# Kernel tuning notes

Hardware: AMD Instinct MI355X
Metric: run time of the kernel (lower is better)

Reference implementation:

```python
import jax, jax.numpy as jnp
import numpy as np
from jax.scipy.special import logsumexp

# Complete binary tree, heap indexing: node i has children 2i+1, 2i+2.
# Edge for child c (c >= 1) is edge_pot[c-1], shape [C, C]:
#   rows = parent state, cols = child state (matches torch code's
#   logsumexp(edge + msg, dim=1) upward and edge.T downward).
DEPTH = 18
C = 16
N = 2 ** (DEPTH + 1) - 1  # 524287 nodes, N-1 edges


def setup_inputs() -> dict:
    key = jax.random.key(0)
    k1, k2 = jax.random.split(key)
    unary = jax.random.normal(k1, (N, C), dtype=jnp.float32)
    edge_pot = jax.random.normal(k2, (N - 1, C, C), dtype=jnp.float32)
    return {"unary": unary, "edge_pot": edge_pot, "depth": DEPTH}


def reference(unary, edge_pot, depth):
    """Sum-product belief propagation on a complete binary tree.

    Returns beliefs [N, C]: for each node v,
      belief[v] = unary[v] + sum(up messages from children) + down message from parent,
    identical to the per-message torch BFS loop, but processed level-parallel.
    """
    c = unary.shape[1]
    # ---------- upward pass (leaves -> root) ----------
    # subtotal[v] = unary[v] + sum of up-messages from v's children (V2F to parent factor)
    subtotal = unary
    m_up = jnp.zeros_like(unary)  # m_up[ch] = F2V message from edge (parent, ch) to parent
    for d in range(depth, 0, -1):
        lo, hi = 2 ** d - 1, 2 ** (d + 1) - 1          # children level, size 2^d
        ep = edge_pot[lo - 1:hi - 1]                    # [2^d, C, C]
        # logsumexp over child state (axis 2): torch's logsumexp(edge + msg, dim=1)
        msg = logsumexp(ep + subtotal[lo:hi][:, None, :], axis=2)  # [2^d, C]
        m_up = m_up.at[lo:hi].set(msg)
        plo, phi = 2 ** (d - 1) - 1, 2 ** d - 1
        # children of consecutive parents are consecutive pairs (2p+1, 2p+2)
        subtotal = subtotal.at[plo:phi].add(msg.reshape(-1, 2, c).sum(axis=1))
    # ---------- downward pass (root -> leaves) ----------
    m_down = jnp.zeros_like(unary)  # m_down[ch] = F2V message from edge (parent, ch) to ch
    for d in range(1, depth + 1):
        lo, hi = 2 ** d - 1, 2 ** (d + 1) - 1
        plo, phi = 2 ** (d - 1) - 1, 2 ** d - 1
        # V2F from parent p towards child ch: all incoming F2V at p except m_up[ch]
        par_total = jnp.repeat(subtotal[plo:phi] + m_down[plo:phi], 2, axis=0)  # [2^d, C]
        v2f = par_total - m_up[lo:hi]
        ep_t = jnp.swapaxes(edge_pot[lo - 1:hi - 1], 1, 2)  # edge.T: [2^d, Cchild, Cparent]
        msg = logsumexp(ep_t + v2f[:, None, :], axis=2)     # logsumexp over parent state
        m_down = m_down.at[lo:hi].set(msg)
    return subtotal + m_down  # beliefs [N, C]
```

## Files before the change

### kernel.cpp

```cpp
#include <hip/hip_runtime.h>
#include <stdint.h>


#ifndef __has_builtin
#define __has_builtin(x) 0
#endif
#if __has_builtin(__builtin_amdgcn_cvt_pk_fp8_f32) && __has_builtin(__builtin_amdgcn_cvt_f32_fp8)
#define EP8_FP8 1
#define EPC_BYTES 256
#else
#define EP8_FP8 0
#define EPC_BYTES 512
#endif

__device__ __forceinline__ void ldvec16(const float* p, float* d) {
    const float4* q = (const float4*)p;
    #pragma unroll
    for (int t = 0; t < 4; ++t) {
        float4 a = q[t];
        d[4*t+0] = a.x; d[4*t+1] = a.y; d[4*t+2] = a.z; d[4*t+3] = a.w;
    }
}

__device__ __forceinline__ float lse16_rs(const float* r, const float* s) {
    float v[16];
    float m;
    #pragma unroll
    for (int j = 0; j < 16; ++j) {
        v[j] = r[j] + s[j];
        m = (j == 0) ? v[0] : fmaxf(m, v[j]);
    }
    float acc = 0.f;
    #pragma unroll
    for (int j = 0; j < 16; ++j) acc += __expf(v[j] - m);
    return m + __logf(acc);
}

__device__ __forceinline__ void enc_row(uint8_t* dst, const float* r) {
#if EP8_FP8
    int w[4];
    #pragma unroll
    for (int t = 0; t < 4; ++t) {
        int x = __builtin_amdgcn_cvt_pk_fp8_f32(r[4*t+0], r[4*t+1], 0, false);
        x     = __builtin_amdgcn_cvt_pk_fp8_f32(r[4*t+2], r[4*t+3], x, true);
        w[t] = x;
    }
    *(int4*)dst = make_int4(w[0], w[1], w[2], w[3]);
#else
    uint32_t w[8];
    #pragma unroll
    for (int t = 0; t < 8; ++t) {
        uint32_t lo = __float_as_uint(r[2*t+0]);
        uint32_t hi = __float_as_uint(r[2*t+1]);
        w[t] = (lo >> 16) | (hi & 0xffff0000u);
    }
    ((int4*)dst)[0] = make_int4(w[0], w[1], w[2], w[3]);
    ((int4*)dst)[1] = make_int4(w[4], w[5], w[6], w[7]);
#endif
}

__device__ __forceinline__ void dec_row(const uint8_t* src, float* r) {
#if EP8_FP8
    uint4 w = *(const uint4*)src;
    uint32_t ws[4] = {w.x, w.y, w.z, w.w};
    #pragma unroll
    for (int t = 0; t < 4; ++t) {
        uint32_t u = ws[t];
        r[4*t+0] = __builtin_amdgcn_cvt_f32_fp8(u, 0);
        r[4*t+1] = __builtin_amdgcn_cvt_f32_fp8(u, 1);
        r[4*t+2] = __builtin_amdgcn_cvt_f32_fp8(u, 2);
        r[4*t+3] = __builtin_amdgcn_cvt_f32_fp8(u, 3);
    }
#else
    uint4 w0 = ((const uint4*)src)[0];
    uint4 w1 = ((const uint4*)src)[1];
    uint32_t ws[8] = {w0.x, w0.y, w0.z, w0.w, w1.x, w1.y, w1.z, w1.w};
    #pragma unroll
    for (int t = 0; t < 8; ++t) {
        r[2*t+0] = __uint_as_float(ws[t] << 16);
        r[2*t+1] = __uint_as_float(ws[t] & 0xffff0000u);
    }
#endif
}

__device__ __forceinline__ float dec_elem(const uint8_t* nodebase, int k, int i) {
#if EP8_FP8
    return __builtin_amdgcn_cvt_f32_fp8((uint32_t)nodebase[k*16 + i], 0);
#else
    uint32_t u = ((const uint16_t*)nodebase)[k*16 + i];
    return __uint_as_float(u << 16);
#endif
}

template <bool WRITE8>
__device__ __forceinline__ void up_body(const float* csrc, const float* __restrict__ unary,
                                        const float* __restrict__ ep, float* out,
                                        uint8_t* __restrict__ e8, int p, int i) {
    int cl = 2*p + 1, cr = cl + 1;
    float s[16], r[16];

    ldvec16(csrc + (size_t)cl*16, s);
    ldvec16(ep + (size_t)(cl-1)*256 + i*16, r);
    float msgL = lse16_rs(r, s);
    if (WRITE8) enc_row(e8 + (size_t)(cl-1)*EPC_BYTES + i*(EPC_BYTES/16), r);

    ldvec16(csrc + (size_t)cr*16, s);
    ldvec16(ep + (size_t)(cr-1)*256 + i*16, r);
    float msgR = lse16_rs(r, s);
    if (WRITE8) enc_row(e8 + (size_t)(cr-1)*EPC_BYTES + i*(EPC_BYTES/16), r);

    out[(size_t)p*16 + i] = unary[(size_t)p*16 + i] + msgL + msgR;
}

template <bool READ8>
__device__ __forceinline__ void down_body(const float* subsrc, const float* __restrict__ ep,
                                          const uint8_t* __restrict__ e8, float* out,
                                          int v, int i) {
    int par = (v - 1) >> 1;
    float s[16], r[16];
    ldvec16(subsrc + (size_t)v*16, s);
    float sub_i = subsrc[(size_t)v*16 + i];

    if (READ8) dec_row(e8 + (size_t)(v-1)*EPC_BYTES + i*(EPC_BYTES/16), r);
    else       ldvec16(ep + (size_t)(v-1)*256 + i*16, r);
    float mup = lse16_rs(r, s);

    float pt  = out[(size_t)par*16 + i];
    float v2f = pt - mup;

    float c[16];
    if (READ8) {
        const uint8_t* nb = e8 + (size_t)(v-1)*EPC_BYTES;
        #pragma unroll
        for (int k = 0; k < 16; ++k) c[k] = dec_elem(nb, k, i);
    } else {
        const float* nb = ep + (size_t)(v-1)*256 + i;
        #pragma unroll
        for (int k = 0; k < 16; ++k) c[k] = nb[k*16];
    }

    float vv[16], m;
    #pragma unroll
    for (int k = 0; k < 16; ++k) {
        float t = c[k] + __shfl(v2f, k, 16);
        vv[k] = t;
        m = (k == 0) ? t : fmaxf(m, t);
    }
    float acc = 0.f;
    #pragma unroll
    for (int k = 0; k < 16; ++k) acc += __expf(vv[k] - m);
    float msg = m + __logf(acc);

    out[(size_t)v*16 + i] = sub_i + msg;
}

template <bool WRITE8>
__global__ __launch_bounds__(256) void up_k(const float* csrc, const float* __restrict__ unary,
                                            const float* __restrict__ ep, float* out,
                                            uint8_t* __restrict__ e8, int plo, int pcount) {
    int t = blockIdx.x * blockDim.x + threadIdx.x;
    if (t >= pcount * 16) return;
    up_body<WRITE8>(csrc, unary, ep, out, e8, plo + (t >> 4), t & 15);
}

template <bool READ8>
__global__ __launch_bounds__(256) void down_k(const float* subsrc, const float* __restrict__ ep,
                                              const uint8_t* __restrict__ e8, float* out,
                                              int lo, int count) {
    int t = blockIdx.x * blockDim.x + threadIdx.x;
    if (t >= count * 16) return;
    down_body<READ8>(subsrc, ep, e8, out, lo + (t >> 4), t & 15);
}

__global__ __launch_bounds__(1024) void top_fused(const float* __restrict__ unary,
                                                  const float* __restrict__ ep,
                                                  float* out, int FD) {
    int tid = threadIdx.x;
    for (int d = FD; d >= 1; --d) {
        int pcount = 1 << (d - 1);
        int plo = pcount - 1;
        int total = pcount * 16;
        for (int t = tid; t < total; t += blockDim.x)
            up_body<false>(out, unary, ep, out, nullptr, plo + (t >> 4), t & 15);
        __syncthreads();
    }
    for (int d = 1; d <= FD; ++d) {
        int count = 1 << d;
        int lo = count - 1;
        int total = count * 16;
        for (int t = tid; t < total; t += blockDim.x)
            down_body<false>(out, ep, nullptr, out, lo + (t >> 4), t & 15);
        __syncthreads();
    }
}

extern "C" void kernel_launch(void* const* d_in, const int* in_sizes, int n_in,
                              void* d_out, int out_size, void* d_ws, size_t ws_size,
                              hipStream_t stream) {
    const float* unary = (const float*)d_in[0];
    const float* ep    = (const float*)d_in[1];
    float* out = (float*)d_out;
    uint8_t* e8 = (uint8_t*)d_ws;

    int Nn = in_sizes[0] / 16;
    int depth = 0;
    while ((1 << (depth + 1)) < Nn + 1) ++depth;

    bool use8 = ws_size >= (size_t)(Nn - 1) * EPC_BYTES;
    int FD = (depth >= 7) ? 6 : 0;

    for (int d = depth; d >= FD + 1; --d) {
        int pcount = 1 << (d - 1);
        int plo = pcount - 1;
        const float* csrc = (d == depth) ? unary : out;
        int threads = pcount * 16;
        dim3 grid((threads + 255) / 256), block(256);
        if (use8) up_k<true ><<<grid, block, 0, stream>>>(csrc, unary, ep, out, e8, plo, pcount);
        else      up_k<false><<<grid, block, 0, stream>>>(csrc, unary, ep, out, e8, plo, pcount);
    }

    if (FD > 0)
        top_fused<<<1, 1024, 0, stream>>>(unary, ep, out, FD);

    for (int d = FD + 1; d <= depth; ++d) {
        int count = 1 << d;
        int lo = count - 1;
        const float* subsrc = (d == depth) ? unary : out;
        int threads = count * 16;
        dim3 grid((threads + 255) / 256), block(256);
        if (use8) down_k<true ><<<grid, block, 0, stream>>>(subsrc, ep, e8, out, lo, count);
        else      down_k<false><<<grid, block, 0, stream>>>(subsrc, ep, e8, out, lo, count);
    }
}
```

Before: 279.8 us.

## Fuse six tree levels per kernel using per-block subtrees with shared-memory handoff

```diff
diff --git a/kernel.cpp b/kernel.cpp
--- a/kernel.cpp
+++ b/kernel.cpp
@@ -92,84 +92,146 @@
 #endif
 }
 
-template <bool WRITE8>
-__device__ __forceinline__ void up_body(const float* csrc, const float* __restrict__ unary,
-                                        const float* __restrict__ ep, float* out,
-                                        uint8_t* __restrict__ e8, int p, int i) {
-    int cl = 2*p + 1, cr = cl + 1;
+template <bool USE8>
+__global__ __launch_bounds__(256) void up_sub(
+    const float* __restrict__ unary, const float* __restrict__ ep,
+    float* __restrict__ out, uint8_t* __restrict__ e8,
+    int rl, int dl, int depth) {
+    __shared__ float sub[2][32][16];
+    int j = blockIdx.x;
+    int cur = 0;
+    for (int d = dl; d > rl; --d) {
+        int np = 1 << (d - 1 - rl);
+        size_t pbase = (((size_t)1 << (d - 1)) - 1) + (size_t)j * np;
+        bool fromGlobal = (d == dl);
+        const float* gsrc = (d == depth) ? unary : out;
+        for (int t = threadIdx.x; t < np * 16; t += 256) {
+            int pl = t >> 4, i = t & 15;
+            size_t p = pbase + pl;
+            size_t cl = 2 * p + 1, cr = cl + 1;
+            float s[16], r[16];
+
+            if (fromGlobal) ldvec16(gsrc + cl * 16, s);
+            else            ldvec16(&sub[cur ^ 1][2 * pl][0], s);
+            ldvec16(ep + (cl - 1) * 256 + i * 16, r);
+            float msgL = lse16_rs(r, s);
+            if (USE8) enc_row(e8 + (cl - 1) * EPC_BYTES + i * (EPC_BYTES / 16), r);
+
+            if (fromGlobal) ldvec16(gsrc + cr * 16, s);
+            else            ldvec16(&sub[cur ^ 1][2 * pl + 1][0], s);
+            ldvec16(ep + (cr - 1) * 256 + i * 16, r);
+            float msgR = lse16_rs(r, s);
+            if (USE8) enc_row(e8 + (cr - 1) * EPC_BYTES + i * (EPC_BYTES / 16), r);
+
+            float v = unary[p * 16 + i] + msgL + msgR;
+            out[p * 16 + i] = v;
+            if (d - 1 > rl) sub[cur][pl][i] = v;
+        }
+        __syncthreads();
+        cur ^= 1;
+    }
+}
+
+template <bool USE8>
+__global__ __launch_bounds__(256) void down_sub(
+    const float* __restrict__ unary, const float* __restrict__ ep,
+    const uint8_t* __restrict__ e8, float* __restrict__ out,
+    int rl, int dl, int depth) {
+    __shared__ float bel[2][32][16];
+    int j = blockIdx.x;
+    int cur = 0;
+    for (int d = rl + 1; d <= dl; ++d) {
+        int nc = 1 << (d - rl);
+        size_t cbase = (((size_t)1 << d) - 1) + (size_t)j * nc;
+        bool leaf = (d == depth);
+        bool parGlobal = (d == rl + 1);
+        for (int t = threadIdx.x; t < nc * 16; t += 256) {
+            int vl = t >> 4, i = t & 15;
+            size_t v = cbase + vl;
+            const float* ssrc = leaf ? unary : out;
+            float s[16], r[16];
+            ldvec16(ssrc + v * 16, s);
+            float sub_i = ssrc[v * 16 + i];
+
+            if (USE8) dec_row(e8 + (v - 1) * EPC_BYTES + i * (EPC_BYTES / 16), r);
+            else      ldvec16(ep + (v - 1) * 256 + i * 16, r);
+            float mup = lse16_rs(r, s);
+
+            float pt;
+            if (parGlobal) pt = out[((v - 1) >> 1) * 16 + i];
+            else           pt = bel[cur ^ 1][vl >> 1][i];
+            float v2f = pt - mup;
+
+            float c[16];
+            if (USE8) {
+                const uint8_t* nb = e8 + (v - 1) * EPC_BYTES;
+                #pragma unroll
+                for (int k = 0; k < 16; ++k) c[k] = dec_elem(nb, k, i);
+            } else {
+                const float* nb = ep + (v - 1) * 256 + i;
+                #pragma unroll
+                for (int k = 0; k < 16; ++k) c[k] = nb[k * 16];
+            }
+
+            float vv[16], m;
+            #pragma unroll
+            for (int k = 0; k < 16; ++k) {
+                float x = c[k] + __shfl(v2f, k, 16);
+                vv[k] = x;
+                m = (k == 0) ? x : fmaxf(m, x);
+            }
+            float acc = 0.f;
+            #pragma unroll
+            for (int k = 0; k < 16; ++k) acc += __expf(vv[k] - m);
+            float msg = m + __logf(acc);
+
+            float b = sub_i + msg;
+            out[v * 16 + i] = b;
+            if (d < dl) bel[cur][vl][i] = b;
+        }
+        __syncthreads();
+        cur ^= 1;
+    }
+}
+
+__device__ __forceinline__ void up_body_f32(const float* __restrict__ unary,
+                                            const float* __restrict__ ep,
+                                            float* out, size_t p, int i) {
+    size_t cl = 2 * p + 1, cr = cl + 1;
     float s[16], r[16];
-
-    ldvec16(csrc + (size_t)cl*16, s);
-    ldvec16(ep + (size_t)(cl-1)*256 + i*16, r);
+    ldvec16(out + cl * 16, s);
+    ldvec16(ep + (cl - 1) * 256 + i * 16, r);
     float msgL = lse16_rs(r, s);
-    if (WRITE8) enc_row(e8 + (size_t)(cl-1)*EPC_BYTES + i*(EPC_BYTES/16), r);
-
-    ldvec16(csrc + (size_t)cr*16, s);
-    ldvec16(ep + (size_t)(cr-1)*256 + i*16, r);
+    ldvec16(out + cr * 16, s);
+    ldvec16(ep + (cr - 1) * 256 + i * 16, r);
     float msgR = lse16_rs(r, s);
-    if (WRITE8) enc_row(e8 + (size_t)(cr-1)*EPC_BYTES + i*(EPC_BYTES/16), r);
-
-    out[(size_t)p*16 + i] = unary[(size_t)p*16 + i] + msgL + msgR;
-}
-
-template <bool READ8>
-__device__ __forceinline__ void down_body(const float* subsrc, const float* __restrict__ ep,
-                                          const uint8_t* __restrict__ e8, float* out,
-                                          int v, int i) {
-    int par = (v - 1) >> 1;
+    out[p * 16 + i] = unary[p * 16 + i] + msgL + msgR;
+}
+
+__device__ __forceinline__ void down_body_f32(const float* __restrict__ ep,
+                                              float* out, size_t v, int i) {
+    size_t par = (v - 1) >> 1;
     float s[16], r[16];
-    ldvec16(subsrc + (size_t)v*16, s);
-    float sub_i = subsrc[(size_t)v*16 + i];
-
-    if (READ8) dec_row(e8 + (size_t)(v-1)*EPC_BYTES + i*(EPC_BYTES/16), r);
-    else       ldvec16(ep + (size_t)(v-1)*256 + i*16, r);
+    ldvec16(out + v * 16, s);
+    float sub_i = out[v * 16 + i];
+    ldvec16(ep + (v - 1) * 256 + i * 16, r);
     float mup = lse16_rs(r, s);
-
-    float pt  = out[(size_t)par*16 + i];
-    float v2f = pt - mup;
-
+    float v2f = out[par * 16 + i] - mup;
+    const float* nb = ep + (v - 1) * 256 + i;
     float c[16];
-    if (READ8) {
-        const uint8_t* nb = e8 + (size_t)(v-1)*EPC_BYTES;
-        #pragma unroll
-        for (int k = 0; k < 16; ++k) c[k] = dec_elem(nb, k, i);
-    } else {
-        const float* nb = ep + (size_t)(v-1)*256 + i;
-        #pragma unroll
-        for (int k = 0; k < 16; ++k) c[k] = nb[k*16];
-    }
-
+    #pragma unroll
+    for (int k = 0; k < 16; ++k) c[k] = nb[k * 16];
     float vv[16], m;
     #pragma unroll
     for (int k = 0; k < 16; ++k) {
-        float t = c[k] + __shfl(v2f, k, 16);
-        vv[k] = t;
-        m = (k == 0) ? t : fmaxf(m, t);
+        float x = c[k] + __shfl(v2f, k, 16);
+        vv[k] = x;
+        m = (k == 0) ? x : fmaxf(m, x);
     }
     float acc = 0.f;
     #pragma unroll
     for (int k = 0; k < 16; ++k) acc += __expf(vv[k] - m);
-    float msg = m + __logf(acc);
-
-    out[(size_t)v*16 + i] = sub_i + msg;
-}
-
-template <bool WRITE8>
-__global__ __launch_bounds__(256) void up_k(const float* csrc, const float* __restrict__ unary,
-                                            const float* __restrict__ ep, float* out,
-                                            uint8_t* __restrict__ e8, int plo, int pcount) {
-    int t = blockIdx.x * blockDim.x + threadIdx.x;
-    if (t >= pcount * 16) return;
-    up_body<WRITE8>(csrc, unary, ep, out, e8, plo + (t >> 4), t & 15);
-}
-
-template <bool READ8>
-__global__ __launch_bounds__(256) void down_k(const float* subsrc, const float* __restrict__ ep,
-                                              const uint8_t* __restrict__ e8, float* out,
-                                              int lo, int count) {
-    int t = blockIdx.x * blockDim.x + threadIdx.x;
-    if (t >= count * 16) return;
-    down_body<READ8>(subsrc, ep, e8, out, lo + (t >> 4), t & 15);
+    out[v * 16 + i] = sub_i + m + __logf(acc);
 }
 
 __global__ __launch_bounds__(1024) void top_fused(const float* __restrict__ unary,
@@ -178,18 +240,16 @@
     int tid = threadIdx.x;
     for (int d = FD; d >= 1; --d) {
         int pcount = 1 << (d - 1);
-        int plo = pcount - 1;
-        int total = pcount * 16;
-        for (int t = tid; t < total; t += blockDim.x)
-            up_body<false>(out, unary, ep, out, nullptr, plo + (t >> 4), t & 15);
+        size_t plo = pcount - 1;
+        for (int t = tid; t < pcount * 16; t += blockDim.x)
+            up_body_f32(unary, ep, out, plo + (t >> 4), t & 15);
         __syncthreads();
     }
     for (int d = 1; d <= FD; ++d) {
         int count = 1 << d;
-        int lo = count - 1;
-        int total = count * 16;
-        for (int t = tid; t < total; t += blockDim.x)
-            down_body<false>(out, ep, nullptr, out, lo + (t >> 4), t & 15);
+        size_t lo = count - 1;
+        for (int t = tid; t < count * 16; t += blockDim.x)
+            down_body_f32(ep, out, lo + (t >> 4), t & 15);
         __syncthreads();
     }
 }
@@ -207,28 +267,26 @@
     while ((1 << (depth + 1)) < Nn + 1) ++depth;
 
     bool use8 = ws_size >= (size_t)(Nn - 1) * EPC_BYTES;
-    int FD = (depth >= 7) ? 6 : 0;
-
-    for (int d = depth; d >= FD + 1; --d) {
-        int pcount = 1 << (d - 1);
-        int plo = pcount - 1;
-        const float* csrc = (d == depth) ? unary : out;
-        int threads = pcount * 16;
-        dim3 grid((threads + 255) / 256), block(256);
-        if (use8) up_k<true ><<<grid, block, 0, stream>>>(csrc, unary, ep, out, e8, plo, pcount);
-        else      up_k<false><<<grid, block, 0, stream>>>(csrc, unary, ep, out, e8, plo, pcount);
-    }
-
+
+    int rls[8], dls[8], nch = 0;
+    int dl = depth;
+    if (depth > 6) {
+        while (dl > 6) { rls[nch] = dl - 6; dls[nch] = dl; ++nch; dl -= 6; }
+    } else {
+        rls[0] = 0; dls[0] = depth; nch = 1; dl = 0;
+    }
+    int FD = dl;
+
+    for (int c = 0; c < nch; ++c) {
+        dim3 grid(1u << rls[c]), block(256);
+        if (use8) up_sub<true ><<<grid, block, 0, stream>>>(unary, ep, out, e8, rls[c], dls[c], depth);
+        else      up_sub<false><<<grid, block, 0, stream>>>(unary, ep, out, e8, rls[c], dls[c], depth);
+    }
     if (FD > 0)
         top_fused<<<1, 1024, 0, stream>>>(unary, ep, out, FD);
-
-    for (int d = FD + 1; d <= depth; ++d) {
-        int count = 1 << d;
-        int lo = count - 1;
-        const float* subsrc = (d == depth) ? unary : out;
-        int threads = count * 16;
-        dim3 grid((threads + 255) / 256), block(256);
-        if (use8) down_k<true ><<<grid, block, 0, stream>>>(subsrc, ep, e8, out, lo, count);
-        else      down_k<false><<<grid, block, 0, stream>>>(subsrc, ep, e8, out, lo, count);
-    }
-}
+    for (int c = nch - 1; c >= 0; --c) {
+        dim3 grid(1u << rls[c]), block(256);
+        if (use8) down_sub<true ><<<grid, block, 0, stream>>>(unary, ep, e8, out, rls[c], dls[c], depth);
+        else      down_sub<false><<<grid, block, 0, stream>>>(unary, ep, e8, out, rls[c], dls[c], depth);
+    }
+}
```

Result: faster. 268.5 us (-4.0%).
